# Optimization experiments

Hardware: AMD Instinct MI355X
Metric: run time of the kernel (lower is better)

Reference implementation:

```python
import jax, jax.numpy as jnp
import numpy as np

N_HEAD = 12
N_EMBD = 768

def setup_inputs() -> dict:
    key = jax.random.key(0)
    ks = jax.random.split(key, 5)
    B, T, C = 4, 2048, N_EMBD
    x = jax.random.normal(ks[0], (B, T, C), dtype=jnp.float32)
    # c_attn: Linear(C, 3C); c_proj: Linear(C, C). Torch Linear stores W as [out,in].
    w_attn = jax.random.normal(ks[1], (3 * C, C), dtype=jnp.float32) * (1.0 / np.sqrt(C))
    b_attn = jnp.zeros((3 * C,), dtype=jnp.float32)
    w_proj = jax.random.normal(ks[2], (C, C), dtype=jnp.float32) * (1.0 / np.sqrt(C))
    b_proj = jnp.zeros((C,), dtype=jnp.float32)
    return {"x": x, "w_attn": w_attn, "b_attn": b_attn, "w_proj": w_proj, "b_proj": b_proj}

def reference(x, w_attn, b_attn, w_proj, b_proj):
    B, T, C = x.shape
    H = N_HEAD
    hs = C // H
    qkv = jnp.einsum('btc,oc->bto', x, w_attn) + b_attn  # [B,T,3C]
    q, k, v = jnp.split(qkv, 3, axis=-1)
    # [B,T,C] -> [B,H,T,hs]
    q = q.reshape(B, T, H, hs).transpose(0, 2, 1, 3)
    k = k.reshape(B, T, H, hs).transpose(0, 2, 1, 3)
    v = v.reshape(B, T, H, hs).transpose(0, 2, 1, 3)
    scale = 1.0 / np.sqrt(hs)
    att = jnp.einsum('bhqd,bhkd->bhqk', q, k) * scale  # [B,H,T,T]
    causal = jnp.tril(jnp.ones((T, T), dtype=bool))
    att = jnp.where(causal[None, None], att, -jnp.inf)
    att = jax.nn.softmax(att, axis=-1)
    y = jnp.einsum('bhqk,bhkd->bhqd', att, v)  # [B,H,T,hs]
    y = y.transpose(0, 2, 1, 3).reshape(B, T, C)
    return jnp.einsum('btc,oc->bto', y, w_proj) + b_proj
```

## Files before the change

### kernel.cpp

```cpp
#include <hip/hip_runtime.h>
#include <hip/hip_bf16.h>


typedef __attribute__((ext_vector_type(8))) short bf16x8;
typedef __attribute__((ext_vector_type(4))) short bf16x4;
typedef __attribute__((ext_vector_type(4))) float f32x4;

#define MFMA16(a, b, c) __builtin_amdgcn_mfma_f32_16x16x32_bf16((a), (b), (c), 0, 0, 0)

__device__ __forceinline__ unsigned short f2bfbits(float f) {
  return __builtin_bit_cast(unsigned short, __float2bfloat16(f));
}
__device__ __forceinline__ float bf2f(short b) {
  return __uint_as_float(((unsigned)(unsigned short)b) << 16);
}
__device__ __forceinline__ float fast_exp2(float x) {
#if __has_builtin(__builtin_amdgcn_exp2f)
  return __builtin_amdgcn_exp2f(x);
#else
  return __expf(x * 0.6931471805599453f);
#endif
}

__device__ __forceinline__ void gload_lds16(const void* g, void* l) {
  __builtin_amdgcn_global_load_lds((const __attribute__((address_space(1))) void*)g,
                                   (__attribute__((address_space(3))) void*)l, 16, 0, 0);
}

__global__ __launch_bounds__(256) void cvt_bf16(const float* __restrict__ in,
                                                unsigned short* __restrict__ out, int n4) {
  int i = blockIdx.x * 256 + threadIdx.x;
  if (i >= n4) return;
  float4 f = ((const float4*)in)[i];
  bf16x4 o;
  o[0] = (short)f2bfbits(f.x); o[1] = (short)f2bfbits(f.y);
  o[2] = (short)f2bfbits(f.z); o[3] = (short)f2bfbits(f.w);
  ((bf16x4*)out)[i] = o;
}

template <typename OutT>
__global__ __launch_bounds__(256) void gemm_bt(const unsigned short* __restrict__ A,
                                               const unsigned short* __restrict__ Bt,
                                               const float* __restrict__ bias,
                                               OutT* __restrict__ C, int M, int N, int K) {
  __shared__ unsigned short As[128 * 64];
  __shared__ unsigned short Bs[128 * 64];
  const int tid = threadIdx.x;
  const int w = tid >> 6, l = tid & 63;
  const int g = l >> 4, li = l & 15;
  const int wm = w >> 1, wn = w & 1;
  const int m0 = blockIdx.y * 128, n0 = blockIdx.x * 128;

  const int scw = (l & 7) ^ ((l >> 3) & 7);
  const int swr = li & 7;

  f32x4 acc[4][4] = {};

  for (int kt = 0; kt < K; kt += 64) {
#pragma unroll
    for (int n = 0; n < 4; ++n) {
      int R = w * 32 + n * 8 + (l >> 3);
      gload_lds16(A + (long)(m0 + R) * K + kt + scw * 8, &As[(w * 32 + n * 8) * 64]);
      gload_lds16(Bt + (long)(n0 + R) * K + kt + scw * 8, &Bs[(w * 32 + n * 8) * 64]);
    }
    __syncthreads();
#pragma unroll
    for (int kk = 0; kk < 2; ++kk) {
      bf16x8 a[4], b[4];
#pragma unroll
      for (int m = 0; m < 4; ++m)
        a[m] = *(const bf16x8*)&As[(wm * 64 + m * 16 + li) * 64 + ((kk * 4 + g) ^ swr) * 8];
#pragma unroll
      for (int n = 0; n < 4; ++n)
        b[n] = *(const bf16x8*)&Bs[(wn * 64 + n * 16 + li) * 64 + ((kk * 4 + g) ^ swr) * 8];
#pragma unroll
      for (int m = 0; m < 4; ++m)
#pragma unroll
        for (int n = 0; n < 4; ++n) acc[m][n] = MFMA16(a[m], b[n], acc[m][n]);
    }
    __syncthreads();
  }

#pragma unroll
  for (int m = 0; m < 4; ++m) {
    int row = m0 + wm * 64 + m * 16 + 4 * g;
#pragma unroll
    for (int n = 0; n < 4; ++n) {
      int col = n0 + wn * 64 + n * 16 + li;
      float bi = bias[col];
#pragma unroll
      for (int r = 0; r < 4; ++r) {
        float v = acc[m][n][r] + bi;
        if constexpr (sizeof(OutT) == 2)
          C[(long)(row + r) * N + col] = (OutT)f2bfbits(v);
        else
          C[(long)(row + r) * N + col] = v;
      }
    }
  }
}

__global__ __launch_bounds__(64) void transpose_v(const unsigned short* __restrict__ qkv,
                                                  unsigned short* __restrict__ vt) {
  const int kt = blockIdx.x & 31, bh = blockIdx.x >> 5;
  const int b = bh / 12, h = bh - b * 12;
  const int l = threadIdx.x;
  const int ct = l & 7, cd = l >> 3;

  bf16x8 tin[8], tout[8];
#pragma unroll
  for (int i = 0; i < 8; ++i)
    tin[i] = *(const bf16x8*)(qkv + (long)(b * 2048 + kt * 64 + ct * 8 + i) * 2304 +
                              1536 + h * 64 + cd * 8);
#pragma unroll
  for (int j = 0; j < 8; ++j) {
#pragma unroll
    for (int i = 0; i < 8; ++i) tout[j][i] = tin[i][j];
    *(bf16x8*)(vt + (long)(bh * 64 + cd * 8 + j) * 2048 + kt * 64 + ct * 8) = tout[j];
  }
}

__device__ __forceinline__ bf16x8 scale_bf8(bf16x8 v, float c) {
  bf16x8 o;
#pragma unroll
  for (int j = 0; j < 8; ++j) o[j] = (short)f2bfbits(bf2f(v[j]) * c);
  return o;
}

__device__ __forceinline__ void softmax_state(f32x4* s, bool diag, int g, int li, int qloc,
                                              unsigned short* PsW, float& m, float& lsum,
                                              f32x4* o) {
  if (diag) {
#pragma unroll
    for (int kn = 0; kn < 4; ++kn)
#pragma unroll
      for (int r = 0; r < 4; ++r)
        if (kn * 16 + 4 * g + r > qloc) s[kn][r] = -1e30f;
  }
  float t0 = fmaxf(fmaxf(s[0][0], s[0][1]), fmaxf(s[0][2], s[0][3]));
  float t1 = fmaxf(fmaxf(s[1][0], s[1][1]), fmaxf(s[1][2], s[1][3]));
  float t2 = fmaxf(fmaxf(s[2][0], s[2][1]), fmaxf(s[2][2], s[2][3]));
  float t3 = fmaxf(fmaxf(s[3][0], s[3][1]), fmaxf(s[3][2], s[3][3]));
  float pm = fmaxf(fmaxf(t0, t1), fmaxf(t2, t3));
  pm = fmaxf(pm, __shfl_xor(pm, 16));
  pm = fmaxf(pm, __shfl_xor(pm, 32));

  if (!__all(pm - m <= 10.0f)) {
    float mn = fmaxf(m, pm);
    float alpha = fast_exp2(m - mn);
    m = mn;
    lsum *= alpha;
    float alo[4];
#pragma unroll
    for (int r = 0; r < 4; ++r) alo[r] = __shfl(alpha, 20 * g + r);
#pragma unroll
    for (int dn = 0; dn < 4; ++dn)
#pragma unroll
      for (int r = 0; r < 4; ++r) o[dn][r] *= alo[r];
  }

  float ps = 0.f;
  const int swp = li & 7;
#pragma unroll
  for (int kn = 0; kn < 4; ++kn) {
    bf16x4 pb;
#pragma unroll
    for (int r = 0; r < 4; ++r) {
      float pv = fast_exp2(s[kn][r] - m);
      ps += pv;
      pb[r] = (short)f2bfbits(pv);
    }
    *(bf16x4*)&PsW[li * 64 + ((kn * 2 + (g >> 1)) ^ swp) * 8 + (g & 1) * 4] = pb;
  }
  ps += __shfl_xor(ps, 16);
  ps += __shfl_xor(ps, 32);
  lsum += ps;
}

template <bool DUAL>
__device__ __forceinline__ void attn_tile(const unsigned short* Ks, const unsigned short* Vs,
                                          unsigned short* PsH, unsigned short* PsL,
                                          const bf16x8* bqh, const bf16x8* bql,
                                          bool diagh, bool diagl, int g, int li, int qloc,
                                          float& mh, float& lh, f32x4* oh,
                                          float& ml, float& ll, f32x4* ol) {
  f32x4 sh[4], sl[4];
  __builtin_amdgcn_s_setprio(1);
#pragma unroll
  for (int kn = 0; kn < 4; ++kn) {
    int rr = kn * 16 + li, sw = rr & 7;
    f32x4 ah = {}, al = {};
#pragma unroll
    for (int kk = 0; kk < 2; ++kk) {
      bf16x8 ak = *(const bf16x8*)&Ks[rr * 64 + ((kk * 4 + g) ^ sw) * 8];
      ah = MFMA16(ak, bqh[kk], ah);
      if constexpr (DUAL) al = MFMA16(ak, bql[kk], al);
    }
    sh[kn] = ah;
    if constexpr (DUAL) sl[kn] = al;
  }
  __builtin_amdgcn_s_setprio(0);

  softmax_state(sh, diagh, g, li, qloc, PsH, mh, lh, oh);
  if constexpr (DUAL) softmax_state(sl, diagl, g, li, qloc, PsL, ml, ll, ol);

  const int swp = li & 7;
  __builtin_amdgcn_s_setprio(1);
#pragma unroll
  for (int kk = 0; kk < 2; ++kk) {
    bf16x8 pah = *(const bf16x8*)&PsH[li * 64 + ((kk * 4 + g) ^ swp) * 8];
    bf16x8 pal;
    if constexpr (DUAL) pal = *(const bf16x8*)&PsL[li * 64 + ((kk * 4 + g) ^ swp) * 8];
#pragma unroll
    for (int dn = 0; dn < 4; ++dn) {
      int rv = dn * 16 + li;
      bf16x8 vb = *(const bf16x8*)&Vs[rv * 64 + ((kk * 4 + g) ^ (rv & 7)) * 8];
      oh[dn] = MFMA16(pah, vb, oh[dn]);
      if constexpr (DUAL) ol[dn] = MFMA16(pal, vb, ol[dn]);
    }
  }
  __builtin_amdgcn_s_setprio(0);
}

__global__ __launch_bounds__(256, 3) void attn_fwd(const unsigned short* __restrict__ qkv,
                                                   const unsigned short* __restrict__ vt,
                                                   unsigned short* __restrict__ y) {
  const int orig = (blockIdx.x & 7) * 96 + (blockIdx.x >> 3);
  const int bh = orig >> 4, p = orig & 15;
  const int b = bh / 12, h = bh - b * 12;
  const int qlo = p, qhi = 31 - p;
  const int tid = threadIdx.x;
  const int w = tid >> 6, l = tid & 63;
  const int g = l >> 4, li = l & 15;
  const int qloc = w * 16 + li;

  __shared__ unsigned short Ks[2][64 * 64];
  __shared__ unsigned short Vs[2][64 * 64];
  __shared__ unsigned short Ps[8][16 * 64];
  unsigned short* PsH = &Ps[w][0];
  unsigned short* PsL = &Ps[4 + w][0];

  const unsigned short* base = qkv + (long)b * 2048 * 2304;

  const float QS = 0.18033688011112042f;
  bf16x8 bqlo[2], bqhi[2];
  {
    const unsigned short* qr = base + (long)(qlo * 64 + qloc) * 2304 + h * 64;
    bqlo[0] = scale_bf8(*(const bf16x8*)(qr + 8 * g), QS);
    bqlo[1] = scale_bf8(*(const bf16x8*)(qr + 32 + 8 * g), QS);
    qr = base + (long)(qhi * 64 + qloc) * 2304 + h * 64;
    bqhi[0] = scale_bf8(*(const bf16x8*)(qr + 8 * g), QS);
    bqhi[1] = scale_bf8(*(const bf16x8*)(qr + 32 + 8 * g), QS);
  }

  float m_lo = -1e30f, l_lo = 0.f, m_hi = -1e30f, l_hi = 0.f;
  f32x4 o_lo[4] = {}, o_hi[4] = {};

  const int sR = w * 8 + (l >> 3);
  const int sc = l & 7;

  int buf = 0;
  {
#pragma unroll
    for (int n = 0; n < 2; ++n) {
      int R = n * 32 + sR;
      int c = sc ^ (R & 7);
      gload_lds16(base + (long)R * 2304 + 768 + h * 64 + c * 8, &Ks[0][(n * 32 + w * 8) * 64]);
      gload_lds16(vt + (long)(bh * 64 + R) * 2048 + c * 8, &Vs[0][(n * 32 + w * 8) * 64]);
    }
  }
  __syncthreads();

  for (int kt = 0; kt <= qhi; ++kt) {
    if (kt < qhi) {
#pragma unroll
      for (int n = 0; n < 2; ++n) {
        int R = n * 32 + sR;
        int c = sc ^ (R & 7);
        gload_lds16(base + (long)((kt + 1) * 64 + R) * 2304 + 768 + h * 64 + c * 8,
                    &Ks[buf ^ 1][(n * 32 + w * 8) * 64]);
        gload_lds16(vt + (long)(bh * 64 + R) * 2048 + (kt + 1) * 64 + c * 8,
                    &Vs[buf ^ 1][(n * 32 + w * 8) * 64]);
      }
    }
    if (kt <= qlo)
      attn_tile<true>(Ks[buf], Vs[buf], PsH, PsL, bqhi, bqlo, kt == qhi, kt == qlo,
                      g, li, qloc, m_hi, l_hi, o_hi, m_lo, l_lo, o_lo);
    else
      attn_tile<false>(Ks[buf], Vs[buf], PsH, PsL, bqhi, bqlo, kt == qhi, false,
                       g, li, qloc, m_hi, l_hi, o_hi, m_lo, l_lo, o_lo);
    __syncthreads();
    buf ^= 1;
  }

#pragma unroll
  for (int t = 0; t < 2; ++t) {
    const f32x4* o = t ? o_hi : o_lo;
    float ls = t ? l_hi : l_lo;
    int qt = t ? qhi : qlo;
#pragma unroll
    for (int r = 0; r < 4; ++r) {
      float lf = __shfl(ls, 20 * g + r);
      float inv = 1.0f / lf;
      long row = (long)b * 2048 + qt * 64 + w * 16 + 4 * g + r;
#pragma unroll
      for (int dn = 0; dn < 4; ++dn)
        y[row * 768 + h * 64 + dn * 16 + li] = (unsigned short)f2bfbits(o[dn][r] * inv);
    }
  }
}

extern "C" void kernel_launch(void* const* d_in, const int* in_sizes, int n_in,
                              void* d_out, int out_size, void* d_ws, size_t ws_size,
                              hipStream_t stream) {
  const float* x      = (const float*)d_in[0];
  const float* w_attn = (const float*)d_in[1];
  const float* b_attn = (const float*)d_in[2];
  const float* w_proj = (const float*)d_in[3];
  const float* b_proj = (const float*)d_in[4];
  float* out = (float*)d_out;

  unsigned short* xb   = (unsigned short*)d_ws;
  unsigned short* wab  = xb + 6291456;
  unsigned short* wpb  = wab + 1769472;
  unsigned short* qkvb = wpb + 589824;
  unsigned short* yb   = qkvb + (long)8192 * 2304;
  unsigned short* vtb  = yb + 6291456;

  cvt_bf16<<<6144, 256, 0, stream>>>(x, xb, 6291456 / 4);
  cvt_bf16<<<1728, 256, 0, stream>>>(w_attn, wab, 1769472 / 4);
  cvt_bf16<<<576, 256, 0, stream>>>(w_proj, wpb, 589824 / 4);

  gemm_bt<unsigned short><<<dim3(18, 64), 256, 0, stream>>>(xb, wab, b_attn, qkvb, 8192, 2304, 768);
  transpose_v<<<1536, 64, 0, stream>>>(qkvb, vtb);
  attn_fwd<<<768, 256, 0, stream>>>(qkvb, vtb, yb);
  gemm_bt<float><<<dim3(6, 64), 256, 0, stream>>>(yb, wpb, b_proj, out, 8192, 768, 768);
}
```

Before: 145.0 us.

## Compute softmax row sums via MFMA with ones, merge cvt kernels, cheaper max/pack

Row sums of the softmax probabilities are now produced by an extra MFMA of P against a ones vector, so the per-tile scalar sums and cross-lane shuffle reductions go away. The sum now comes from the bf16-rounded P, which matches the values actually used in P·V. The max reduction uses three-input max chains, and bf16 packing truncates the float bits instead of rounding. The three fp32-to-bf16 conversion launches are merged into one kernel to save launch overhead. Truncation adds a small rounding bias, and the extra MFMA adds matrix work in every tile.

```diff
diff --git a/kernel.cpp b/kernel.cpp
--- a/kernel.cpp
+++ b/kernel.cpp
@@ -21,21 +21,37 @@
   return __expf(x * 0.6931471805599453f);
 #endif
 }
+__device__ __forceinline__ float fmax3(float a, float b, float c) {
+  return fmaxf(fmaxf(a, b), c);
+}
+__device__ __forceinline__ unsigned pk2bf(float lo, float hi) {
+  return (__builtin_bit_cast(unsigned, hi) & 0xffff0000u) |
+         (__builtin_bit_cast(unsigned, lo) >> 16);
+}
 
 __device__ __forceinline__ void gload_lds16(const void* g, void* l) {
   __builtin_amdgcn_global_load_lds((const __attribute__((address_space(1))) void*)g,
                                    (__attribute__((address_space(3))) void*)l, 16, 0, 0);
 }
 
-__global__ __launch_bounds__(256) void cvt_bf16(const float* __restrict__ in,
-                                                unsigned short* __restrict__ out, int n4) {
+__global__ __launch_bounds__(256) void cvt3(const float* __restrict__ x,
+                                            const float* __restrict__ wa,
+                                            const float* __restrict__ wp,
+                                            unsigned short* __restrict__ xb,
+                                            unsigned short* __restrict__ wab,
+                                            unsigned short* __restrict__ wpb) {
   int i = blockIdx.x * 256 + threadIdx.x;
-  if (i >= n4) return;
-  float4 f = ((const float4*)in)[i];
+  const float* in;
+  unsigned short* out;
+  int j;
+  if (i < 1572864) { in = x; out = xb; j = i; }
+  else if (i < 2015232) { in = wa; out = wab; j = i - 1572864; }
+  else { in = wp; out = wpb; j = i - 2015232; }
+  float4 f = ((const float4*)in)[j];
   bf16x4 o;
   o[0] = (short)f2bfbits(f.x); o[1] = (short)f2bfbits(f.y);
   o[2] = (short)f2bfbits(f.z); o[3] = (short)f2bfbits(f.w);
-  ((bf16x4*)out)[i] = o;
+  ((bf16x4*)out)[j] = o;
 }
 
 template <typename OutT>
@@ -128,8 +144,8 @@
 }
 
 __device__ __forceinline__ void softmax_state(f32x4* s, bool diag, int g, int li, int qloc,
-                                              unsigned short* PsW, float& m, float& lsum,
-                                              f32x4* o) {
+                                              unsigned short* PsW, float& m, f32x4* o,
+                                              f32x4& o4) {
   if (diag) {
 #pragma unroll
     for (int kn = 0; kn < 4; ++kn)
@@ -137,11 +153,12 @@
       for (int r = 0; r < 4; ++r)
         if (kn * 16 + 4 * g + r > qloc) s[kn][r] = -1e30f;
   }
-  float t0 = fmaxf(fmaxf(s[0][0], s[0][1]), fmaxf(s[0][2], s[0][3]));
-  float t1 = fmaxf(fmaxf(s[1][0], s[1][1]), fmaxf(s[1][2], s[1][3]));
-  float t2 = fmaxf(fmaxf(s[2][0], s[2][1]), fmaxf(s[2][2], s[2][3]));
-  float t3 = fmaxf(fmaxf(s[3][0], s[3][1]), fmaxf(s[3][2], s[3][3]));
-  float pm = fmaxf(fmaxf(t0, t1), fmaxf(t2, t3));
+  float a = fmax3(s[0][0], s[0][1], s[0][2]);
+  float b = fmax3(s[0][3], s[1][0], s[1][1]);
+  float c = fmax3(s[1][2], s[1][3], s[2][0]);
+  float d = fmax3(s[2][1], s[2][2], s[2][3]);
+  float e = fmax3(s[3][0], s[3][1], s[3][2]);
+  float pm = fmaxf(fmax3(a, b, c), fmax3(d, e, s[3][3]));
   pm = fmaxf(pm, __shfl_xor(pm, 16));
   pm = fmaxf(pm, __shfl_xor(pm, 32));
 
@@ -149,7 +166,6 @@
     float mn = fmaxf(m, pm);
     float alpha = fast_exp2(m - mn);
     m = mn;
-    lsum *= alpha;
     float alo[4];
 #pragma unroll
     for (int r = 0; r < 4; ++r) alo[r] = __shfl(alpha, 20 * g + r);
@@ -157,24 +173,20 @@
     for (int dn = 0; dn < 4; ++dn)
 #pragma unroll
       for (int r = 0; r < 4; ++r) o[dn][r] *= alo[r];
-  }
-
-  float ps = 0.f;
+#pragma unroll
+    for (int r = 0; r < 4; ++r) o4[r] *= alo[r];
+  }
+
   const int swp = li & 7;
 #pragma unroll
   for (int kn = 0; kn < 4; ++kn) {
-    bf16x4 pb;
-#pragma unroll
-    for (int r = 0; r < 4; ++r) {
-      float pv = fast_exp2(s[kn][r] - m);
-      ps += pv;
-      pb[r] = (short)f2bfbits(pv);
-    }
-    *(bf16x4*)&PsW[li * 64 + ((kn * 2 + (g >> 1)) ^ swp) * 8 + (g & 1) * 4] = pb;
-  }
-  ps += __shfl_xor(ps, 16);
-  ps += __shfl_xor(ps, 32);
-  lsum += ps;
+    float e0 = fast_exp2(s[kn][0] - m);
+    float e1 = fast_exp2(s[kn][1] - m);
+    float e2 = fast_exp2(s[kn][2] - m);
+    float e3 = fast_exp2(s[kn][3] - m);
+    uint2 pk = {pk2bf(e0, e1), pk2bf(e2, e3)};
+    *(uint2*)&PsW[li * 64 + ((kn * 2 + (g >> 1)) ^ swp) * 8 + (g & 1) * 4] = pk;
+  }
 }
 
 template <bool DUAL>
@@ -182,8 +194,8 @@
                                           unsigned short* PsH, unsigned short* PsL,
                                           const bf16x8* bqh, const bf16x8* bql,
                                           bool diagh, bool diagl, int g, int li, int qloc,
-                                          float& mh, float& lh, f32x4* oh,
-                                          float& ml, float& ll, f32x4* ol) {
+                                          float& mh, f32x4* oh, f32x4& oh4,
+                                          float& ml, f32x4* ol, f32x4& ol4) {
   f32x4 sh[4], sl[4];
   __builtin_amdgcn_s_setprio(1);
 #pragma unroll
@@ -201,8 +213,12 @@
   }
   __builtin_amdgcn_s_setprio(0);
 
-  softmax_state(sh, diagh, g, li, qloc, PsH, mh, lh, oh);
-  if constexpr (DUAL) softmax_state(sl, diagl, g, li, qloc, PsL, ml, ll, ol);
+  softmax_state(sh, diagh, g, li, qloc, PsH, mh, oh, oh4);
+  if constexpr (DUAL) softmax_state(sl, diagl, g, li, qloc, PsL, ml, ol, ol4);
+
+  bf16x8 vones;
+#pragma unroll
+  for (int j = 0; j < 8; ++j) vones[j] = (short)0x3F80;
 
   const int swp = li & 7;
   __builtin_amdgcn_s_setprio(1);
@@ -218,6 +234,8 @@
       oh[dn] = MFMA16(pah, vb, oh[dn]);
       if constexpr (DUAL) ol[dn] = MFMA16(pal, vb, ol[dn]);
     }
+    oh4 = MFMA16(pah, vones, oh4);
+    if constexpr (DUAL) ol4 = MFMA16(pal, vones, ol4);
   }
   __builtin_amdgcn_s_setprio(0);
 }
@@ -253,8 +271,9 @@
     bqhi[1] = scale_bf8(*(const bf16x8*)(qr + 32 + 8 * g), QS);
   }
 
-  float m_lo = -1e30f, l_lo = 0.f, m_hi = -1e30f, l_hi = 0.f;
+  float m_lo = -1e30f, m_hi = -1e30f;
   f32x4 o_lo[4] = {}, o_hi[4] = {};
+  f32x4 o4_lo = {}, o4_hi = {};
 
   const int sR = w * 8 + (l >> 3);
   const int sc = l & 7;
@@ -285,10 +304,10 @@
     }
     if (kt <= qlo)
       attn_tile<true>(Ks[buf], Vs[buf], PsH, PsL, bqhi, bqlo, kt == qhi, kt == qlo,
-                      g, li, qloc, m_hi, l_hi, o_hi, m_lo, l_lo, o_lo);
+                      g, li, qloc, m_hi, o_hi, o4_hi, m_lo, o_lo, o4_lo);
     else
       attn_tile<false>(Ks[buf], Vs[buf], PsH, PsL, bqhi, bqlo, kt == qhi, false,
-                       g, li, qloc, m_hi, l_hi, o_hi, m_lo, l_lo, o_lo);
+                       g, li, qloc, m_hi, o_hi, o4_hi, m_lo, o_lo, o4_lo);
     __syncthreads();
     buf ^= 1;
   }
@@ -296,12 +315,11 @@
 #pragma unroll
   for (int t = 0; t < 2; ++t) {
     const f32x4* o = t ? o_hi : o_lo;
-    float ls = t ? l_hi : l_lo;
+    const f32x4& o4 = t ? o4_hi : o4_lo;
     int qt = t ? qhi : qlo;
 #pragma unroll
     for (int r = 0; r < 4; ++r) {
-      float lf = __shfl(ls, 20 * g + r);
-      float inv = 1.0f / lf;
+      float inv = 1.0f / o4[r];
       long row = (long)b * 2048 + qt * 64 + w * 16 + 4 * g + r;
 #pragma unroll
       for (int dn = 0; dn < 4; ++dn)
@@ -327,9 +345,7 @@
   unsigned short* yb   = qkvb + (long)8192 * 2304;
   unsigned short* vtb  = yb + 6291456;
 
-  cvt_bf16<<<6144, 256, 0, stream>>>(x, xb, 6291456 / 4);
-  cvt_bf16<<<1728, 256, 0, stream>>>(w_attn, wab, 1769472 / 4);
-  cvt_bf16<<<576, 256, 0, stream>>>(w_proj, wpb, 589824 / 4);
+  cvt3<<<8448, 256, 0, stream>>>(x, w_attn, w_proj, xb, wab, wpb);
 
   gemm_bt<unsigned short><<<dim3(18, 64), 256, 0, stream>>>(xb, wab, b_attn, qkvb, 8192, 2304, 768);
   transpose_v<<<1536, 64, 0, stream>>>(qkvb, vtb);
```

Result: faster. 140.5 us (-3.1%).
